# Kernel optimization log

Hardware: AMD Instinct MI355X
Metric: run time of the kernel (lower is better)

Reference implementation:

```python
import jax, jax.numpy as jnp
import numpy as np

HEAD_SIZE = 128  # hidden_size 2048 / 16 heads; used only as softmax scale in this module


def setup_inputs() -> dict:
    key = jax.random.key(0)
    ks = jax.random.split(key, 4)
    B, S, H = 2, 4096, 2048
    hidden_states = jax.random.normal(ks[0], (B, S, H), dtype=jnp.float32)
    attention_mask = jnp.zeros((B, 1, S), dtype=jnp.float32)  # additive mask, broadcasts onto [B,S,S]
    s = 1.0 / np.sqrt(H)
    Wq = jax.random.normal(ks[1], (H, H), dtype=jnp.float32) * s
    Wk = jax.random.normal(ks[2], (H, H), dtype=jnp.float32) * s
    Wv = jax.random.normal(ks[3], (H, H), dtype=jnp.float32) * s
    bq = jnp.zeros((H,), dtype=jnp.float32)
    bk = jnp.zeros((H,), dtype=jnp.float32)
    bv = jnp.zeros((H,), dtype=jnp.float32)
    return {"hidden_states": hidden_states, "attention_mask": attention_mask,
            "Wq": Wq, "bq": bq, "Wk": Wk, "bk": bk, "Wv": Wv, "bv": bv}


def reference(hidden_states, attention_mask, Wq, bq, Wk, bk, Wv, bv):
    # Self-attention: cross_hidden_states defaults to hidden_states.
    q = jnp.einsum('bsh,oh->bso', hidden_states, Wq) + bq  # [B,S,H]
    k = jnp.einsum('bsh,oh->bso', hidden_states, Wk) + bk
    v = jnp.einsum('bsh,oh->bso', hidden_states, Wv) + bv
    # Note: module never splits heads, so scores are a single [B,S,S] matrix
    scores = jnp.einsum('bqh,bkh->bqk', q, k) / jnp.sqrt(jnp.asarray(HEAD_SIZE, q.dtype))
    scores = scores + attention_mask  # additive mask, broadcast
    probs = jax.nn.softmax(scores, axis=-1)  # dropout p=0 -> identity
    context = jnp.einsum('bqk,bkh->bqh', probs, v)  # [B,S,H]
    return context
```

## Files before the change

kernel.cpp:

```cpp
#include <hip/hip_runtime.h>

typedef _Float16 f16;
typedef _Float16 f16x8 __attribute__((ext_vector_type(8)));
typedef _Float16 f16x4 __attribute__((ext_vector_type(4)));
typedef float    f32x4 __attribute__((ext_vector_type(4)));

#define GLD16(g, l)                                                            \
  __builtin_amdgcn_global_load_lds(                                            \
      (const __attribute__((address_space(1))) void*)(g),                      \
      (__attribute__((address_space(3))) void*)(l), 16, 0, 0)

static constexpr int S = 4096, H = 2048, B = 2;

__global__ __launch_bounds__(256) void cast_all(
    const float* __restrict__ hs, const float* __restrict__ w0,
    const float* __restrict__ w1, const float* __restrict__ w2,
    f16* __restrict__ hs_h, f16* __restrict__ w_h) {
  const int hsN4 = B * S * H / 4;
  const int wN4  = H * H / 4;
  int i = blockIdx.x * 256 + threadIdx.x;
  float4 f;
  if (i < hsN4) {
    f = reinterpret_cast<const float4*>(hs)[i];
    f16x4 h = {(f16)f.x, (f16)f.y, (f16)f.z, (f16)f.w};
    reinterpret_cast<f16x4*>(hs_h)[i] = h;
  } else {
    int j = i - hsN4;
    int seg = j / wN4, off = j - seg * wN4;
    const float* src = seg == 0 ? w0 : (seg == 1 ? w1 : w2);
    f = reinterpret_cast<const float4*>(src)[off];
    f16x4 h = {(f16)f.x, (f16)f.y, (f16)f.z, (f16)f.w};
    reinterpret_cast<f16x4*>(w_h)[j] = h;
  }
}

template <int MODE>
__global__ __launch_bounds__(512, 2) void gemm_tn(
    const f16* __restrict__ A, const f16* __restrict__ Bm,
    void* __restrict__ C0, void* __restrict__ C1, void* __restrict__ C2,
    const float* __restrict__ x0, const float* __restrict__ x1,
    const float* __restrict__ x2, float scale, int K, int lda, int ldb) {
  __shared__ __attribute__((aligned(16))) char smem[131072];

  const int tileM = blockIdx.y * 256;
  const int tileN = blockIdx.x * 256;

  const int tid  = threadIdx.x;
  const int wave = tid >> 6, lane = tid & 63;
  const int wm = (wave >> 2) * 128;
  const int wn = (wave & 3) * 64;
  const int ln = lane & 15, kq = lane >> 4;

  f32x4 acc[8][4] = {};

  size_t rowB = tileN;
  if (MODE == 2) rowB = (size_t)(tileM >> 12) * S + tileN;
  if (MODE == 3) rowB = (size_t)(tileM >> 12) * H + tileN;
  const f16* gA = A + (size_t)tileM * lda;
  const f16* gB = Bm + rowB * ldb;

  int aoff[4], boff[4], loff[4];
#pragma unroll
  for (int j = 0; j < 4; ++j) {
    int id = j * 512 + tid;
    int r = id >> 3, cs = (id & 7) ^ (r & 7) ^ ((r & 16) >> 2);
    aoff[j] = r * lda + cs * 8;
    boff[j] = r * ldb + cs * 8;
    loff[j] = id * 8;
  }

  const int nt = K >> 6;

  auto rdfrag = [&](const f16* sT, int rbase, int ks) -> f16x8 {
    const int row = rbase + ln;
    const int slot = (ks * 4 + kq) ^ (row & 7) ^ ((row & 16) >> 2);
    return *reinterpret_cast<const f16x8*>(&sT[row * 64 + slot * 8]);
  };

  {
    f16* pA = (f16*)smem;
    f16* pB = (f16*)(smem + 32768);
#pragma unroll
    for (int j = 0; j < 4; ++j) GLD16(gA + aoff[j], &pA[loff[j]]);
#pragma unroll
    for (int j = 0; j < 4; ++j) GLD16(gB + boff[j], &pB[loff[j]]);
  }
  asm volatile("s_waitcnt vmcnt(0)" ::: "memory");
  __builtin_amdgcn_s_barrier();

  for (int t = 0; t < nt; ++t) {
    const int cur = t & 1;
    const f16* sA = (const f16*)(smem + cur * 65536);
    const f16* sB = (const f16*)(smem + cur * 65536 + 32768);
    f16* pA = (f16*)(smem + (cur ^ 1) * 65536);
    f16* pB = (f16*)(smem + (cur ^ 1) * 65536 + 32768);
    const int kg = (t + 1) * 64;
    const bool pf = (t + 1 < nt);

    f16x8 bf[2][4];

#pragma unroll
    for (int ks = 0; ks < 2; ++ks)
#pragma unroll
      for (int y = 0; y < 4; ++y) bf[ks][y] = rdfrag(sB, wn + y * 16, ks);
    f16x8 a00 = rdfrag(sA, wm + 0 * 16, 0), a01 = rdfrag(sA, wm + 0 * 16, 1);
    f16x8 a10 = rdfrag(sA, wm + 1 * 16, 0), a11 = rdfrag(sA, wm + 1 * 16, 1);
    if (pf) {
#pragma unroll
      for (int j = 0; j < 4; ++j) GLD16(gA + aoff[j] + kg, &pA[loff[j]]);
#pragma unroll
      for (int j = 0; j < 4; ++j) GLD16(gB + boff[j] + kg, &pB[loff[j]]);
    }
    __builtin_amdgcn_s_barrier();
    asm volatile("s_waitcnt lgkmcnt(0)" ::: "memory");
    __builtin_amdgcn_sched_barrier(0);
    __builtin_amdgcn_s_setprio(1);
#pragma unroll
    for (int y = 0; y < 4; ++y) {
      acc[0][y] = __builtin_amdgcn_mfma_f32_16x16x32_f16(a00, bf[0][y], acc[0][y], 0, 0, 0);
      acc[1][y] = __builtin_amdgcn_mfma_f32_16x16x32_f16(a10, bf[0][y], acc[1][y], 0, 0, 0);
    }
#pragma unroll
    for (int y = 0; y < 4; ++y) {
      acc[0][y] = __builtin_amdgcn_mfma_f32_16x16x32_f16(a01, bf[1][y], acc[0][y], 0, 0, 0);
      acc[1][y] = __builtin_amdgcn_mfma_f32_16x16x32_f16(a11, bf[1][y], acc[1][y], 0, 0, 0);
    }
    __builtin_amdgcn_s_setprio(0);
    __builtin_amdgcn_s_barrier();

#pragma unroll
    for (int p = 1; p < 4; ++p) {
      f16x8 b00 = rdfrag(sA, wm + (2 * p + 0) * 16, 0);
      f16x8 b01 = rdfrag(sA, wm + (2 * p + 0) * 16, 1);
      f16x8 b10 = rdfrag(sA, wm + (2 * p + 1) * 16, 0);
      f16x8 b11 = rdfrag(sA, wm + (2 * p + 1) * 16, 1);
      __builtin_amdgcn_s_barrier();
      asm volatile("s_waitcnt lgkmcnt(0)" ::: "memory");
      __builtin_amdgcn_sched_barrier(0);
      __builtin_amdgcn_s_setprio(1);
#pragma unroll
      for (int y = 0; y < 4; ++y) {
        acc[2 * p + 0][y] = __builtin_amdgcn_mfma_f32_16x16x32_f16(b00, bf[0][y], acc[2 * p + 0][y], 0, 0, 0);
        acc[2 * p + 1][y] = __builtin_amdgcn_mfma_f32_16x16x32_f16(b10, bf[0][y], acc[2 * p + 1][y], 0, 0, 0);
      }
#pragma unroll
      for (int y = 0; y < 4; ++y) {
        acc[2 * p + 0][y] = __builtin_amdgcn_mfma_f32_16x16x32_f16(b01, bf[1][y], acc[2 * p + 0][y], 0, 0, 0);
        acc[2 * p + 1][y] = __builtin_amdgcn_mfma_f32_16x16x32_f16(b11, bf[1][y], acc[2 * p + 1][y], 0, 0, 0);
      }
      __builtin_amdgcn_s_setprio(0);
      if (p == 3 && pf)
        asm volatile("s_waitcnt vmcnt(0)" ::: "memory");
      __builtin_amdgcn_s_barrier();
    }
  }

  if (MODE == 0 && (tileN >> 11) == 2) {
    const int nn0 = tileN - 2 * H;
    const int b = tileM >> 12, s0 = tileM & (S - 1);
    f16* sT = (f16*)smem;
#pragma unroll
    for (int p = 0; p < 4; ++p) {
      if ((wave & 3) == p) {
#pragma unroll
        for (int x = 0; x < 8; ++x)
#pragma unroll
          for (int y = 0; y < 4; ++y) {
            int scol = y * 16 + ln;
            float bias = x2[nn0 + p * 64 + scol];
            int row0 = wm + x * 16 + kq * 4;
            f16x4 h4 = {(f16)(acc[x][y][0] + bias), (f16)(acc[x][y][1] + bias),
                        (f16)(acc[x][y][2] + bias), (f16)(acc[x][y][3] + bias)};
            *reinterpret_cast<f16x4*>(&sT[scol * 264 + row0]) = h4;
          }
      }
      __syncthreads();
      {
        int c = tid >> 3, hh = tid & 7;
        const f16* src = &sT[c * 264 + hh * 32];
        f16* dst = (f16*)C2 + (size_t)b * H * S + (size_t)(nn0 + p * 64 + c) * S +
                   s0 + hh * 32;
#pragma unroll
        for (int j = 0; j < 4; ++j)
          reinterpret_cast<f16x8*>(dst)[j] = reinterpret_cast<const f16x8*>(src)[j];
      }
      __syncthreads();
    }
    return;
  }

#pragma unroll
  for (int x = 0; x < 8; ++x)
#pragma unroll
    for (int y = 0; y < 4; ++y)
#pragma unroll
      for (int r = 0; r < 4; ++r) {
        int m = tileM + wm + x * 16 + kq * 4 + r;
        int n = tileN + wn + y * 16 + ln;
        float v = acc[x][y][r];
        if (MODE == 0) {
          int seg = n >> 11, nn = n & 2047;
          if (seg == 0) {
            ((f16*)C0)[(size_t)m * H + nn] = (f16)(v + x0[nn]);
          } else {
            ((f16*)C1)[(size_t)m * H + nn] = (f16)(v + x1[nn]);
          }
        } else if (MODE == 2) {
          int b = m >> 12;
          ((f16*)C0)[(size_t)m * S + n] = (f16)(v * scale + x0[(size_t)b * S + n]);
        } else {
          ((float*)C0)[(size_t)m * H + n] = v;
        }
      }
}

__global__ __launch_bounds__(256) void softmax_f16(f16* __restrict__ sc) {
  const int tid = threadIdx.x;
  f16* rp = sc + (size_t)blockIdx.x * S;
  f16x8 h[2];
#pragma unroll
  for (int j = 0; j < 2; ++j) h[j] = reinterpret_cast<f16x8*>(rp)[tid + j * 256];

  float v[16];
#pragma unroll
  for (int j = 0; j < 2; ++j)
#pragma unroll
    for (int e = 0; e < 8; ++e) v[j * 8 + e] = (float)h[j][e];

  float m = -1e30f;
#pragma unroll
  for (int e = 0; e < 16; ++e) m = fmaxf(m, v[e]);
#pragma unroll
  for (int off = 32; off; off >>= 1) m = fmaxf(m, __shfl_xor(m, off));

  __shared__ float red[8];
  int wave = tid >> 6, lane = tid & 63;
  if (lane == 0) red[wave] = m;
  __syncthreads();
  m = fmaxf(fmaxf(red[0], red[1]), fmaxf(red[2], red[3]));

  float s = 0.f;
#pragma unroll
  for (int e = 0; e < 16; ++e) { v[e] = __expf(v[e] - m); s += v[e]; }
#pragma unroll
  for (int off = 32; off; off >>= 1) s += __shfl_xor(s, off);
  if (lane == 0) red[4 + wave] = s;
  __syncthreads();
  s = red[4] + red[5] + red[6] + red[7];
  float inv = 1.0f / s;

#pragma unroll
  for (int j = 0; j < 2; ++j) {
#pragma unroll
    for (int e = 0; e < 8; ++e) h[j][e] = (f16)(v[j * 8 + e] * inv);
    reinterpret_cast<f16x8*>(rp)[tid + j * 256] = h[j];
  }
}

extern "C" void kernel_launch(void* const* d_in, const int* in_sizes, int n_in,
                              void* d_out, int out_size, void* d_ws, size_t ws_size,
                              hipStream_t stream) {
  const float* hs   = (const float*)d_in[0];
  const float* mask = (const float*)d_in[1];
  const float* Wq   = (const float*)d_in[2];
  const float* bq   = (const float*)d_in[3];
  const float* Wk   = (const float*)d_in[4];
  const float* bk   = (const float*)d_in[5];
  const float* Wv   = (const float*)d_in[6];
  const float* bv   = (const float*)d_in[7];
  float* out = (float*)d_out;

  f16* hs_h = (f16*)d_ws;
  f16* w_h  = hs_h + (size_t)B * S * H;
  f16* Qh   = w_h + (size_t)3 * H * H;
  f16* Kh   = Qh + (size_t)B * S * H;
  f16* Vt   = Kh + (size_t)B * S * H;
  f16* Sc   = Vt + (size_t)B * S * H;

  const int castN = B * S * H / 4 + 3 * H * H / 4;
  cast_all<<<(castN + 255) / 256, 256, 0, stream>>>(hs, Wq, Wk, Wv, hs_h, w_h);

  dim3 blk(512);
  const float sscale = 0.088388347648318447f;

  gemm_tn<0><<<dim3(24, 32), blk, 0, stream>>>(
      hs_h, w_h, Qh, Kh, Vt, bq, bk, bv, 1.f, H, H, H);

  gemm_tn<2><<<dim3(16, 32), blk, 0, stream>>>(
      Qh, Kh, Sc, nullptr, nullptr, mask, nullptr, nullptr, sscale, H, H, H);

  softmax_f16<<<B * S, 256, 0, stream>>>(Sc);

  gemm_tn<3><<<dim3(8, 32), blk, 0, stream>>>(
      Sc, Vt, out, nullptr, nullptr, nullptr, nullptr, nullptr, 1.f, S, S, S);
}
```

Measured before the change: 630.5 us.

## Replace double-buffered GEMM K-tiles with a five-slot half-tile ring

The GEMM mainloop moves from two full 256x64 A/B buffers to a five-slot ring of 128-row half-tiles, raising LDS to 160 KB. Loads for later half-tiles are spread across the four compute phases of each iteration, and partial vmcnt waits replace the full drain before each barrier. Each wave reads only the half-tile slot that holds its rows. The aim is to keep more global loads in flight and hide load latency behind MFMA work, at the cost of more LDS and more complex slot and wait bookkeeping.

```diff
diff --git a/kernel.cpp b/kernel.cpp
--- a/kernel.cpp
+++ b/kernel.cpp
@@ -40,7 +40,7 @@
     void* __restrict__ C0, void* __restrict__ C1, void* __restrict__ C2,
     const float* __restrict__ x0, const float* __restrict__ x1,
     const float* __restrict__ x2, float scale, int K, int lda, int ldb) {
-  __shared__ __attribute__((aligned(16))) char smem[131072];
+  __shared__ __attribute__((aligned(16))) char smem[163840];
 
   const int tileM = blockIdx.y * 256;
   const int tileN = blockIdx.x * 256;
@@ -59,100 +59,98 @@
   const f16* gA = A + (size_t)tileM * lda;
   const f16* gB = Bm + rowB * ldb;
 
-  int aoff[4], boff[4], loff[4];
-#pragma unroll
-  for (int j = 0; j < 4; ++j) {
+  int aoffL[2], boffL[2], loffL[2];
+#pragma unroll
+  for (int j = 0; j < 2; ++j) {
     int id = j * 512 + tid;
-    int r = id >> 3, cs = (id & 7) ^ (r & 7) ^ ((r & 16) >> 2);
-    aoff[j] = r * lda + cs * 8;
-    boff[j] = r * ldb + cs * 8;
-    loff[j] = id * 8;
+    int r = id >> 3;
+    int cs = (id & 7) ^ (r & 7) ^ ((r & 16) >> 2);
+    aoffL[j] = r * lda + cs * 8;
+    boffL[j] = r * ldb + cs * 8;
+    loffL[j] = id * 8;
   }
 
   const int nt = K >> 6;
 
-  auto rdfrag = [&](const f16* sT, int rbase, int ks) -> f16x8 {
-    const int row = rbase + ln;
+  auto stageA = [&](int h, int buf) {
+    f16* d = (f16*)(smem + buf * 32768);
+    const f16* s = gA + (size_t)((h & 1) * 128) * lda + (size_t)(h >> 1) * 64;
+#pragma unroll
+    for (int j = 0; j < 2; ++j) GLD16(s + aoffL[j], d + loffL[j]);
+  };
+  auto stageB = [&](int h, int buf) {
+    f16* d = (f16*)(smem + buf * 32768 + 16384);
+    const f16* s = gB + (size_t)((h & 1) * 128) * ldb + (size_t)(h >> 1) * 64;
+#pragma unroll
+    for (int j = 0; j < 2; ++j) GLD16(s + boffL[j], d + loffL[j]);
+  };
+
+  auto rdfrag = [&](const f16* base, int rloc, int ks) -> f16x8 {
+    const int row = rloc + ln;
     const int slot = (ks * 4 + kq) ^ (row & 7) ^ ((row & 16) >> 2);
-    return *reinterpret_cast<const f16x8*>(&sT[row * 64 + slot * 8]);
+    return *reinterpret_cast<const f16x8*>(&base[row * 64 + slot * 8]);
   };
 
-  {
-    f16* pA = (f16*)smem;
-    f16* pB = (f16*)(smem + 32768);
-#pragma unroll
-    for (int j = 0; j < 4; ++j) GLD16(gA + aoff[j], &pA[loff[j]]);
-#pragma unroll
-    for (int j = 0; j < 4; ++j) GLD16(gB + boff[j], &pB[loff[j]]);
-  }
-  asm volatile("s_waitcnt vmcnt(0)" ::: "memory");
+  stageA(0, 0); stageB(0, 0);
+  stageA(1, 1); stageB(1, 1);
+  stageA(2, 2); stageB(2, 2);
+  asm volatile("s_waitcnt vmcnt(4)" ::: "memory");
   __builtin_amdgcn_s_barrier();
 
+  const int ahalf = wm >> 7, bhalf = wn >> 7;
+  int c0 = 0;
   for (int t = 0; t < nt; ++t) {
-    const int cur = t & 1;
-    const f16* sA = (const f16*)(smem + cur * 65536);
-    const f16* sB = (const f16*)(smem + cur * 65536 + 32768);
-    f16* pA = (f16*)(smem + (cur ^ 1) * 65536);
-    f16* pB = (f16*)(smem + (cur ^ 1) * 65536 + 32768);
-    const int kg = (t + 1) * 64;
-    const bool pf = (t + 1 < nt);
+    int bA = c0 + ahalf; if (bA >= 5) bA -= 5;
+    int bB = c0 + bhalf; if (bB >= 5) bB -= 5;
+    const f16* sAw = (const f16*)(smem + bA * 32768);
+    const f16* sBw = (const f16*)(smem + bB * 32768 + 16384);
+    int s3 = c0 + 3; if (s3 >= 5) s3 -= 5;
+    int s4 = c0 + 4; if (s4 >= 5) s4 -= 5;
+    const int h3 = 2 * t + 3, h4 = 2 * t + 4;
+    const bool pf3 = h3 < 2 * nt, pf4 = h4 < 2 * nt;
 
     f16x8 bf[2][4];
 
 #pragma unroll
-    for (int ks = 0; ks < 2; ++ks)
-#pragma unroll
-      for (int y = 0; y < 4; ++y) bf[ks][y] = rdfrag(sB, wn + y * 16, ks);
-    f16x8 a00 = rdfrag(sA, wm + 0 * 16, 0), a01 = rdfrag(sA, wm + 0 * 16, 1);
-    f16x8 a10 = rdfrag(sA, wm + 1 * 16, 0), a11 = rdfrag(sA, wm + 1 * 16, 1);
-    if (pf) {
-#pragma unroll
-      for (int j = 0; j < 4; ++j) GLD16(gA + aoff[j] + kg, &pA[loff[j]]);
-#pragma unroll
-      for (int j = 0; j < 4; ++j) GLD16(gB + boff[j] + kg, &pB[loff[j]]);
-    }
-    __builtin_amdgcn_s_barrier();
-    asm volatile("s_waitcnt lgkmcnt(0)" ::: "memory");
-    __builtin_amdgcn_sched_barrier(0);
-    __builtin_amdgcn_s_setprio(1);
-#pragma unroll
-    for (int y = 0; y < 4; ++y) {
-      acc[0][y] = __builtin_amdgcn_mfma_f32_16x16x32_f16(a00, bf[0][y], acc[0][y], 0, 0, 0);
-      acc[1][y] = __builtin_amdgcn_mfma_f32_16x16x32_f16(a10, bf[0][y], acc[1][y], 0, 0, 0);
-    }
-#pragma unroll
-    for (int y = 0; y < 4; ++y) {
-      acc[0][y] = __builtin_amdgcn_mfma_f32_16x16x32_f16(a01, bf[1][y], acc[0][y], 0, 0, 0);
-      acc[1][y] = __builtin_amdgcn_mfma_f32_16x16x32_f16(a11, bf[1][y], acc[1][y], 0, 0, 0);
-    }
-    __builtin_amdgcn_s_setprio(0);
-    __builtin_amdgcn_s_barrier();
-
-#pragma unroll
-    for (int p = 1; p < 4; ++p) {
-      f16x8 b00 = rdfrag(sA, wm + (2 * p + 0) * 16, 0);
-      f16x8 b01 = rdfrag(sA, wm + (2 * p + 0) * 16, 1);
-      f16x8 b10 = rdfrag(sA, wm + (2 * p + 1) * 16, 0);
-      f16x8 b11 = rdfrag(sA, wm + (2 * p + 1) * 16, 1);
+    for (int p = 0; p < 4; ++p) {
+      if (p == 0) {
+#pragma unroll
+        for (int ks = 0; ks < 2; ++ks)
+#pragma unroll
+          for (int y = 0; y < 4; ++y)
+            bf[ks][y] = rdfrag(sBw, (wn & 64) + y * 16, ks);
+      }
+      f16x8 a00 = rdfrag(sAw, (2 * p + 0) * 16, 0);
+      f16x8 a01 = rdfrag(sAw, (2 * p + 0) * 16, 1);
+      f16x8 a10 = rdfrag(sAw, (2 * p + 1) * 16, 0);
+      f16x8 a11 = rdfrag(sAw, (2 * p + 1) * 16, 1);
+      if (p == 0 && pf3) stageA(h3, s3);
+      if (p == 1 && pf3) stageB(h3, s3);
+      if (p == 2 && pf4) stageA(h4, s4);
+      if (p == 3 && pf4) stageB(h4, s4);
+      if (p == 0) asm volatile("s_waitcnt lgkmcnt(8)" ::: "memory");
       __builtin_amdgcn_s_barrier();
       asm volatile("s_waitcnt lgkmcnt(0)" ::: "memory");
       __builtin_amdgcn_sched_barrier(0);
       __builtin_amdgcn_s_setprio(1);
 #pragma unroll
       for (int y = 0; y < 4; ++y) {
-        acc[2 * p + 0][y] = __builtin_amdgcn_mfma_f32_16x16x32_f16(b00, bf[0][y], acc[2 * p + 0][y], 0, 0, 0);
-        acc[2 * p + 1][y] = __builtin_amdgcn_mfma_f32_16x16x32_f16(b10, bf[0][y], acc[2 * p + 1][y], 0, 0, 0);
+        acc[2 * p + 0][y] = __builtin_amdgcn_mfma_f32_16x16x32_f16(a00, bf[0][y], acc[2 * p + 0][y], 0, 0, 0);
+        acc[2 * p + 1][y] = __builtin_amdgcn_mfma_f32_16x16x32_f16(a10, bf[0][y], acc[2 * p + 1][y], 0, 0, 0);
       }
 #pragma unroll
       for (int y = 0; y < 4; ++y) {
-        acc[2 * p + 0][y] = __builtin_amdgcn_mfma_f32_16x16x32_f16(b01, bf[1][y], acc[2 * p + 0][y], 0, 0, 0);
-        acc[2 * p + 1][y] = __builtin_amdgcn_mfma_f32_16x16x32_f16(b11, bf[1][y], acc[2 * p + 1][y], 0, 0, 0);
+        acc[2 * p + 0][y] = __builtin_amdgcn_mfma_f32_16x16x32_f16(a01, bf[1][y], acc[2 * p + 0][y], 0, 0, 0);
+        acc[2 * p + 1][y] = __builtin_amdgcn_mfma_f32_16x16x32_f16(a11, bf[1][y], acc[2 * p + 1][y], 0, 0, 0);
       }
       __builtin_amdgcn_s_setprio(0);
-      if (p == 3 && pf)
-        asm volatile("s_waitcnt vmcnt(0)" ::: "memory");
+      if (p == 3) {
+        if (pf4) asm volatile("s_waitcnt vmcnt(4)" ::: "memory");
+        else     asm volatile("s_waitcnt vmcnt(0)" ::: "memory");
+      }
       __builtin_amdgcn_s_barrier();
     }
+    c0 += 2; if (c0 >= 5) c0 -= 5;
   }
 
   if (MODE == 0 && (tileN >> 11) == 2) {
```

After: 630.6 us. About the same (+0.0%).
